# Kernel tuning notes

Hardware: AMD Instinct MI355X
Metric: run time of the kernel (lower is better)

## Reference

```python
import jax, jax.numpy as jnp
import numpy as np

EPS = 1e-6
H = 16

def setup_inputs() -> dict:
    key = jax.random.key(0)
    ks = jax.random.split(key, 11)
    B, L, D = 4, 4096, 1024
    sc = 1.0 / np.sqrt(D)
    return {
        "queries": jax.random.normal(ks[0], (B, L, D), jnp.float32),
        "keys": jax.random.normal(ks[1], (B, L, D), jnp.float32),
        "values": jax.random.normal(ks[2], (B, L, D), jnp.float32),
        "Wq": jax.random.normal(ks[3], (D, D), jnp.float32) * sc,
        "bq": jax.random.normal(ks[4], (D,), jnp.float32) * 0.01,
        "Wk": jax.random.normal(ks[5], (D, D), jnp.float32) * sc,
        "bk": jax.random.normal(ks[6], (D,), jnp.float32) * 0.01,
        "Wv": jax.random.normal(ks[7], (D, D), jnp.float32) * sc,
        "bv": jax.random.normal(ks[8], (D,), jnp.float32) * 0.01,
        "Wo": jax.random.normal(ks[9], (D, D), jnp.float32) * sc,
        "bo": jax.random.normal(ks[10], (D,), jnp.float32) * 0.01,
    }

def reference(queries, keys, values, Wq, bq, Wk, bk, Wv, bv, Wo, bo):
    B, L, _ = queries.shape
    S = keys.shape[1]
    # projections + split heads: [B, H, L, dh]
    q = (queries @ Wq + bq).reshape(B, L, H, -1).transpose(0, 2, 1, 3)
    k = (keys @ Wk + bk).reshape(B, S, H, -1).transpose(0, 2, 1, 3)
    v = (values @ Wv + bv).reshape(B, S, H, -1).transpose(0, 2, 1, 3)
    # kernel feature map
    q = jax.nn.sigmoid(q)
    k = jax.nn.sigmoid(k)
    # flow normalization (sink/source)
    sink_incoming = 1.0 / jnp.einsum('nhld,nhd->nhl', q + EPS, k.sum(axis=2) + EPS)
    source_outgoing = 1.0 / jnp.einsum('nhld,nhd->nhl', k + EPS, q.sum(axis=2) + EPS)
    conserved_sink = jnp.einsum('nhld,nhd->nhl', q + EPS,
                                (k * source_outgoing[..., None]).sum(axis=2) + EPS)
    conserved_source = jnp.einsum('nhld,nhd->nhl', k + EPS,
                                  (q * sink_incoming[..., None]).sum(axis=2) + EPS)
    conserved_source = jnp.clip(conserved_source, -1.0, 1.0)
    sink_allocation = jax.nn.sigmoid(conserved_sink * (float(L) / float(S)))
    source_competition = jax.nn.softmax(conserved_source, axis=-1) * float(S)
    # linear attention: kv then q(kv)
    qn = q * sink_incoming[..., None]
    vn = v * source_competition[..., None]
    kv = jnp.einsum('nhld,nhlm->nhdm', k, vn)
    x = jnp.einsum('nhld,nhdm->nhlm', qn, kv) * sink_allocation[..., None]
    x = x.transpose(0, 2, 1, 3).reshape(B, L, -1)
    return x @ Wo + bo
```

## Files before the change

### kernel.cpp

```cpp
#include <hip/hip_runtime.h>

#define Bc 4
#define Lc 4096
#define Dc 1024
#define LDQ 3072
#define Mc (Bc*Lc)
#define EPSc 1e-6f

typedef __bf16 bf16x8 __attribute__((ext_vector_type(8)));
typedef __bf16 bf16x4 __attribute__((ext_vector_type(4)));
typedef float f32x4 __attribute__((ext_vector_type(4)));

typedef __attribute__((address_space(3))) void lds_vt;
typedef const __attribute__((address_space(1))) void gbl_vt;

__device__ __forceinline__ void gll16(const void* g, void* l) {
  __builtin_amdgcn_global_load_lds((gbl_vt*)g, (lds_vt*)l, 16, 0, 0);
}

__global__ __launch_bounds__(256) void conv3(const float* __restrict__ Q, const float* __restrict__ K,
                                             const float* __restrict__ V, __bf16* __restrict__ Y) {
  const float* src = (blockIdx.y == 0) ? Q : (blockIdx.y == 1) ? K : V;
  __bf16* dst = Y + (size_t)blockIdx.y * ((size_t)Mc * Dc);
  const int i = blockIdx.x * 256 + threadIdx.x;
  const float4 v = ((const float4*)src)[i];
  bf16x4 o;
  o[0] = (__bf16)v.x; o[1] = (__bf16)v.y; o[2] = (__bf16)v.z; o[3] = (__bf16)v.w;
  ((bf16x4*)dst)[i] = o;
}

__global__ __launch_bounds__(256) void wt_conv4(const float* __restrict__ W0, const float* __restrict__ W1,
                                                const float* __restrict__ W2, const float* __restrict__ W3,
                                                __bf16* __restrict__ T) {
  const float* W = (blockIdx.z == 0) ? W0 : (blockIdx.z == 1) ? W1 : (blockIdx.z == 2) ? W2 : W3;
  __bf16* Wt = T + (size_t)blockIdx.z * ((size_t)Dc * Dc);
  __shared__ float t[32][33];
  const int n0 = blockIdx.x << 5, k0 = blockIdx.y << 5;
  const int tx = threadIdx.x, ty = threadIdx.y;
#pragma unroll
  for (int i = 0; i < 4; ++i)
    t[ty + 8 * i][tx] = W[(size_t)(k0 + ty + 8 * i) * Dc + n0 + tx];
  __syncthreads();
#pragma unroll
  for (int i = 0; i < 4; ++i)
    Wt[(size_t)(n0 + ty + 8 * i) * Dc + k0 + tx] = (__bf16)t[tx][ty + 8 * i];
}

template <int FUSED>
__global__ __launch_bounds__(256, 2) void gemm256x128(
    const __bf16* __restrict__ Aq_, const __bf16* __restrict__ Ak_, const __bf16* __restrict__ Av_,
    const __bf16* __restrict__ Wq_, const __bf16* __restrict__ Wk_, const __bf16* __restrict__ Wv_,
    const float* __restrict__ bq_, const float* __restrict__ bk_, const float* __restrict__ bv_,
    void* __restrict__ Cp, float* __restrict__ qsum, float* __restrict__ ksum) {
  __shared__ __bf16 As[256 * 32];
  __shared__ __bf16 Bs[128 * 32];
  const int tid = threadIdx.x;
  const int lane = tid & 63, w4 = tid >> 6;
  const int wr = w4 >> 1, wc = w4 & 1;
  const int lf = lane & 15, kq = lane >> 4;

  constexpr int NCT = FUSED ? 24 : 8;
  constexpr int CPX = (64 * NCT) >> 3;
  const int hwlin = blockIdx.x + blockIdx.y * 64;
  const int swz = (hwlin & 7) * CPX + (hwlin >> 3);
  const int bx = swz / NCT, ct = swz - bx * NCT;
  const int row0 = bx << 8, col0 = ct << 7;
  const int region = FUSED ? (ct >> 3) : 0;
  const int colL = FUSED ? (col0 & 1023) : col0;

  const __bf16* Agl = FUSED ? (region == 0 ? Aq_ : (region == 1 ? Ak_ : Av_)) : Aq_;
  const __bf16* Bgl = FUSED ? (region == 0 ? Wq_ : (region == 1 ? Wk_ : Wv_)) : Wq_;
  const float* biasp = FUSED ? (region == 0 ? bq_ : (region == 1 ? bk_ : bv_)) : bq_;
  const __bf16* Ab_g = Agl + (size_t)row0 * 1024;
  const __bf16* Bb_g = Bgl + (size_t)colL * 1024;

  int arow[4], asrc[4];
#pragma unroll
  for (int i = 0; i < 4; ++i) {
    const int g = i * 256 + tid;
    arow[i] = g >> 2;
    asrc[i] = ((g & 3) ^ ((arow[i] >> 1) & 3)) << 3;
  }
  const int kgsw = (kq ^ ((lf >> 1) & 3)) << 3;
  const int arb = (wr * 128 + lf) * 32 + kgsw;
  const int brb = (wc * 64 + lf) * 32 + kgsw;

  f32x4 acc[8][4] = {};

  for (int t = 0; t < 32; ++t) {
    const int kb = t << 5;
#pragma unroll
    for (int i = 0; i < 4; ++i)
      gll16(Ab_g + (size_t)arow[i] * 1024 + kb + asrc[i], &As[(i * 256 + tid) * 8]);
#pragma unroll
    for (int i = 0; i < 2; ++i)
      gll16(Bb_g + (size_t)arow[i] * 1024 + kb + asrc[i], &Bs[(i * 256 + tid) * 8]);
    __syncthreads();
    bf16x8 af[8], bfr[4];
#pragma unroll
    for (int m = 0; m < 8; ++m) af[m] = *(const bf16x8*)(As + arb + m * 512);
#pragma unroll
    for (int n = 0; n < 4; ++n) bfr[n] = *(const bf16x8*)(Bs + brb + n * 512);
#pragma unroll
    for (int m = 0; m < 8; ++m)
#pragma unroll
      for (int n = 0; n < 4; ++n)
        acc[m][n] = __builtin_amdgcn_mfma_f32_16x16x32_bf16(bfr[n], af[m], acc[m][n], 0, 0, 0);
    __syncthreads();
  }

  const int b_of = row0 >> 12;
  const int orow = row0 + wr * 128 + lf;
  const int ocl = wc * 64 + (kq << 2);
#pragma unroll
  for (int n = 0; n < 4; ++n) {
    const int cl = ocl + (n << 4);
    const int cb = colL + cl;
    const f32x4 bb = *(const f32x4*)&biasp[cb];
    f32x4 sacc = {0.f, 0.f, 0.f, 0.f};
#pragma unroll
    for (int m = 0; m < 8; ++m) {
      f32x4 v = acc[m][n] + bb;
      if (FUSED && region < 2) {
#pragma unroll
        for (int r = 0; r < 4; ++r) v[r] = 1.0f / (1.0f + expf(-v[r]));
      }
      if (FUSED) {
        bf16x4 o;
#pragma unroll
        for (int r = 0; r < 4; ++r) o[r] = (__bf16)v[r];
        *(bf16x4*)&((__bf16*)Cp)[(size_t)(orow + (m << 4)) * LDQ + col0 + cl] = o;
      } else {
        *(f32x4*)&((float*)Cp)[(size_t)(orow + (m << 4)) * 1024 + col0 + cl] = v;
      }
      sacc += v;
    }
    if (FUSED && region < 2) {
#pragma unroll
      for (int o = 1; o < 16; o <<= 1) {
        sacc[0] += __shfl_xor(sacc[0], o); sacc[1] += __shfl_xor(sacc[1], o);
        sacc[2] += __shfl_xor(sacc[2], o); sacc[3] += __shfl_xor(sacc[3], o);
      }
      if (lf == 0) {
        float* sums = (region == 0) ? qsum : ksum;
#pragma unroll
        for (int r = 0; r < 4; ++r) atomicAdd(&sums[b_of * 1024 + cb + r], sacc[r]);
      }
    }
  }
}

__global__ __launch_bounds__(256) void r2_flow(const __bf16* __restrict__ Qp, const __bf16* __restrict__ Kp,
                                               const float* __restrict__ ksum, const float* __restrict__ qsum,
                                               float* __restrict__ si,
                                               float* __restrict__ qsi, float* __restrict__ kso) {
  const int blk = blockIdx.x;
  const int chunk = blk & 15, bh = blk >> 4;
  const int b = bh >> 4, h = bh & 15;
  const int d = threadIdx.x & 63, w = threadIdx.x >> 6;
  __shared__ float ksE[64], qsE[64];
  if (threadIdx.x < 64) ksE[threadIdx.x] = ksum[bh * 64 + threadIdx.x] + EPSc;
  else if (threadIdx.x < 128) qsE[threadIdx.x - 64] = qsum[bh * 64 + threadIdx.x - 64] + EPSc;
  __syncthreads();
  const float kE = ksE[d], qE = qsE[d];
  const size_t base = ((size_t)b * Lc) * LDQ + h * 64 + d;
  const size_t obase = (size_t)bh * Lc;
  float qsia = 0.f, ksoa = 0.f;
  const int l0 = chunk * 256;
  for (int i = w; i < 256; i += 4) {
    const int l = l0 + i;
    const size_t idx = base + (size_t)l * LDQ;
    const float qv = (float)Qp[idx], kvv = (float)Kp[idx];
    float a = (qv + EPSc) * kE;
    float c2 = (kvv + EPSc) * qE;
#pragma unroll
    for (int o = 32; o; o >>= 1) { a += __shfl_xor(a, o); c2 += __shfl_xor(c2, o); }
    const float sil = 1.0f / a, sol = 1.0f / c2;
    if (d == 0) si[obase + l] = sil;
    qsia += qv * sil;
    ksoa += kvv * sol;
  }
  atomicAdd(&qsi[bh * 64 + d], qsia);
  atomicAdd(&kso[bh * 64 + d], ksoa);
}

__global__ __launch_bounds__(256) void r3_cons(const __bf16* __restrict__ Qp, const __bf16* __restrict__ Kp,
                                               const float* __restrict__ qsi, const float* __restrict__ kso,
                                               float* __restrict__ sa, float* __restrict__ csx,
                                               float* __restrict__ den) {
  const int blk = blockIdx.x;
  const int chunk = blk & 15, bh = blk >> 4;
  const int b = bh >> 4, h = bh & 15;
  const int d = threadIdx.x & 63, w = threadIdx.x >> 6;
  __shared__ float ksoE[64], qsiE[64];
  if (threadIdx.x < 64) ksoE[threadIdx.x] = kso[bh * 64 + threadIdx.x] + EPSc;
  else if (threadIdx.x < 128) qsiE[threadIdx.x - 64] = qsi[bh * 64 + threadIdx.x - 64] + EPSc;
  __syncthreads();
  const float kE = ksoE[d], qE = qsiE[d];
  const size_t base = ((size_t)b * Lc) * LDQ + h * 64 + d;
  const size_t obase = (size_t)bh * Lc;
  const int l0 = chunk * 256;
  float eacc = 0.f;
  for (int i = w; i < 256; i += 4) {
    const int l = l0 + i;
    const size_t idx = base + (size_t)l * LDQ;
    const float qv = (float)Qp[idx], kvv = (float)Kp[idx];
    float a = (qv + EPSc) * kE;
    float c2 = (kvv + EPSc) * qE;
#pragma unroll
    for (int o = 32; o; o >>= 1) { a += __shfl_xor(a, o); c2 += __shfl_xor(c2, o); }
    if (d == 0) {
      sa[obase + l] = 1.0f / (1.0f + expf(-a));
      const float cl = fminf(1.0f, fmaxf(-1.0f, c2));
      const float e = expf(cl);
      csx[obase + l] = e;
      eacc += e;
    }
  }
  if (d == 0) atomicAdd(&den[bh], eacc);
}

__global__ __launch_bounds__(256) void k5_kv(const __bf16* __restrict__ Kp, const __bf16* __restrict__ Vp,
                                             const float* __restrict__ csx, const float* __restrict__ den,
                                             float* __restrict__ kvout) {
  const int bh = blockIdx.x, chunk = blockIdx.y;
  const int b = bh >> 4, h = bh & 15;
  const int tid = threadIdx.x;
  const int dq = (tid >> 4) << 2;
  const int mq = (tid & 15) << 2;
  const float sden = 4096.0f / den[bh];
  __shared__ float klds[4][64], vlds[4][64];
  float acc[4][4] = {};
  const int r = tid >> 6, c = tid & 63;
  const size_t rowbase = ((size_t)b * Lc + chunk * 512) * LDQ + h * 64;
  const size_t csbase = (size_t)bh * Lc + chunk * 512;
  for (int i = 0; i < 512; i += 4) {
    const size_t idx = rowbase + (size_t)(i + r) * LDQ + c;
    const float sc = csx[csbase + i + r] * sden;
    klds[r][c] = (float)Kp[idx];
    vlds[r][c] = (float)Vp[idx] * sc;
    __syncthreads();
#pragma unroll
    for (int rr = 0; rr < 4; ++rr) {
      float kr[4], vr[4];
#pragma unroll
      for (int j = 0; j < 4; ++j) { kr[j] = klds[rr][dq + j]; vr[j] = vlds[rr][mq + j]; }
#pragma unroll
      for (int a = 0; a < 4; ++a)
#pragma unroll
        for (int e = 0; e < 4; ++e) acc[a][e] += kr[a] * vr[e];
    }
    __syncthreads();
  }
#pragma unroll
  for (int a = 0; a < 4; ++a)
#pragma unroll
    for (int e = 0; e < 4; ++e)
      atomicAdd(&kvout[(size_t)bh * 4096 + (dq + a) * 64 + mq + e], acc[a][e]);
}

__global__ __launch_bounds__(256) void k6_x(const __bf16* __restrict__ Qp,
                                            const float* __restrict__ kvin, const float* __restrict__ si,
                                            const float* __restrict__ sa, __bf16* __restrict__ Xb) {
  const int bh = blockIdx.x, chunk = blockIdx.y;
  const int b = bh >> 4, h = bh & 15;
  const int tid = threadIdx.x, lane = tid & 63, w = tid >> 6;
  const int lf = lane & 15, kq = lane >> 4;
  __shared__ float ktl[64][66];
  for (int e = tid; e < 4096; e += 256)
    ktl[e & 63][e >> 6] = kvin[(size_t)bh * 4096 + e];
  __syncthreads();
  bf16x8 kh[4][2], kl[4][2];
#pragma unroll
  for (int mi = 0; mi < 4; ++mi)
#pragma unroll
    for (int hf = 0; hf < 2; ++hf) {
      const float* p = &ktl[mi * 16 + lf][hf * 32 + kq * 8];
      bf16x8 hi, lo;
#pragma unroll
      for (int j = 0; j < 8; ++j) {
        const float f = p[j];
        hi[j] = (__bf16)f;
        lo[j] = (__bf16)(f - (float)hi[j]);
      }
      kh[mi][hf] = hi; kl[mi][hf] = lo;
    }
  const size_t bL = (size_t)b * Lc;
  const size_t obase = (size_t)bh * Lc;
#pragma unroll
  for (int gi = 0; gi < 4; ++gi) {
    const int lrow = chunk * 256 + (w * 4 + gi) * 16 + lf;
    const size_t qb = (bL + lrow) * LDQ + h * 64;
    const bf16x8 qf0 = *(const bf16x8*)(Qp + qb + kq * 8);
    const bf16x8 qf1 = *(const bf16x8*)(Qp + qb + 32 + kq * 8);
    const float sc = si[obase + lrow] * sa[obase + lrow];
    f32x4 acc[4] = {};
#pragma unroll
    for (int mi = 0; mi < 4; ++mi) {
      acc[mi] = __builtin_amdgcn_mfma_f32_16x16x32_bf16(kh[mi][0], qf0, acc[mi], 0, 0, 0);
      acc[mi] = __builtin_amdgcn_mfma_f32_16x16x32_bf16(kh[mi][1], qf1, acc[mi], 0, 0, 0);
      acc[mi] = __builtin_amdgcn_mfma_f32_16x16x32_bf16(kl[mi][0], qf0, acc[mi], 0, 0, 0);
      acc[mi] = __builtin_amdgcn_mfma_f32_16x16x32_bf16(kl[mi][1], qf1, acc[mi], 0, 0, 0);
    }
#pragma unroll
    for (int mi = 0; mi < 4; ++mi) {
      bf16x4 o;
#pragma unroll
      for (int r = 0; r < 4; ++r) o[r] = (__bf16)(acc[mi][r] * sc);
      *(bf16x4*)&Xb[(bL + lrow) * Dc + h * 64 + mi * 16 + (kq << 2)] = o;
    }
  }
}

extern "C" void kernel_launch(void* const* d_in, const int* in_sizes, int n_in,
                              void* d_out, int out_size, void* d_ws, size_t ws_size,
                              hipStream_t stream) {
  const float* Qin = (const float*)d_in[0];
  const float* Kin = (const float*)d_in[1];
  const float* Vin = (const float*)d_in[2];
  const float* Wq = (const float*)d_in[3];
  const float* bq = (const float*)d_in[4];
  const float* Wk = (const float*)d_in[5];
  const float* bk = (const float*)d_in[6];
  const float* Wv = (const float*)d_in[7];
  const float* bv = (const float*)d_in[8];
  const float* Wo = (const float*)d_in[9];
  const float* bo = (const float*)d_in[10];

  const size_t MD = (size_t)Mc * Dc;
  __bf16* Aq = (__bf16*)d_ws;
  __bf16* Ak = Aq + MD;
  __bf16* Av = Ak + MD;
  __bf16* Wqt = Av + MD;
  __bf16* Wkt = Wqt + (size_t)Dc * Dc;
  __bf16* Wvt = Wkt + (size_t)Dc * Dc;
  __bf16* Wot = Wvt + (size_t)Dc * Dc;
  __bf16* QKV = Wot + (size_t)Dc * Dc;
  float* F = (float*)(QKV + (size_t)Mc * LDQ);
  float* ksum = F;
  float* qsum = ksum + 4096;
  float* kso = qsum + 4096;
  float* qsi = kso + 4096;
  float* den = qsi + 4096;
  float* kv = den + 64;
  float* si = kv + 262144;
  float* sa = si + 262144;
  float* csx = sa + 262144;
  __bf16* Xb = Aq;

  hipMemsetAsync(F, 0, (size_t)(4 * 4096 + 64 + 262144) * sizeof(float), stream);

  conv3<<<dim3((int)(MD / 4 / 256), 3), 256, 0, stream>>>(Qin, Kin, Vin, Aq);
  wt_conv4<<<dim3(32, 32, 4), dim3(32, 8), 0, stream>>>(Wq, Wk, Wv, Wo, Wqt);

  gemm256x128<1><<<dim3(64, 24), 256, 0, stream>>>(Aq, Ak, Av, Wqt, Wkt, Wvt,
                                                   bq, bk, bv, QKV, qsum, ksum);

  const __bf16* Qp = QKV;
  const __bf16* Kp = QKV + 1024;
  const __bf16* Vp = QKV + 2048;
  r2_flow<<<1024, 256, 0, stream>>>(Qp, Kp, ksum, qsum, si, qsi, kso);
  r3_cons<<<1024, 256, 0, stream>>>(Qp, Kp, qsi, kso, sa, csx, den);
  k5_kv<<<dim3(64, 8), 256, 0, stream>>>(Kp, Vp, csx, den, kv);
  k6_x<<<dim3(64, 16), 256, 0, stream>>>(Qp, kv, si, sa, Xb);

  gemm256x128<0><<<dim3(64, 8), 256, 0, stream>>>(Xb, nullptr, nullptr, Wot, nullptr, nullptr,
                                                  bo, nullptr, nullptr, d_out, nullptr, nullptr);
}
```

Baseline: 490.6 us.

## Use 128x128 tiles with 64-wide K steps for fused QKV projection GEMM

Adds a new GEMM kernel with 128x128 output tiles and a 64-deep K step per loop iteration, loaded as two 32-wide LDS halves, with a launch bound of 4 blocks per CU. The fused QKV projection now uses it instead of the 256x128 kernel. The grid doubles to 3072 blocks and each iteration issues more loads per barrier, aiming at higher occupancy, better wave balance across CUs and fewer syncs. The trade-off is less operand reuse per block and twice as many atomic column-sum updates.

```diff
diff --git a/kernel.cpp b/kernel.cpp
--- a/kernel.cpp
+++ b/kernel.cpp
@@ -44,6 +44,116 @@
 #pragma unroll
   for (int i = 0; i < 4; ++i)
     Wt[(size_t)(n0 + ty + 8 * i) * Dc + k0 + tx] = (__bf16)t[tx][ty + 8 * i];
+}
+
+template <int FUSED>
+__global__ __launch_bounds__(256, 4) void gemm128b(
+    const __bf16* __restrict__ Aq_, const __bf16* __restrict__ Ak_, const __bf16* __restrict__ Av_,
+    const __bf16* __restrict__ Wq_, const __bf16* __restrict__ Wk_, const __bf16* __restrict__ Wv_,
+    const float* __restrict__ bq_, const float* __restrict__ bk_, const float* __restrict__ bv_,
+    void* __restrict__ Cp, float* __restrict__ qsum, float* __restrict__ ksum) {
+  __shared__ __bf16 As[2][128 * 32];
+  __shared__ __bf16 Bs[2][128 * 32];
+  const int tid = threadIdx.x;
+  const int lane = tid & 63, w4 = tid >> 6;
+  const int wr = w4 >> 1, wc = w4 & 1;
+  const int lf = lane & 15, kq = lane >> 4;
+
+  constexpr int NCT = FUSED ? 24 : 8;
+  constexpr int CPX = (128 * NCT) >> 3;
+  const int hwlin = blockIdx.x + (blockIdx.y << 7);
+  const int swz = (hwlin & 7) * CPX + (hwlin >> 3);
+  const int bx = swz / NCT, ct = swz - bx * NCT;
+  const int row0 = bx << 7, col0 = ct << 7;
+  const int region = FUSED ? (ct >> 3) : 0;
+  const int colL = FUSED ? (col0 & 1023) : col0;
+
+  const __bf16* Agl = FUSED ? (region == 0 ? Aq_ : (region == 1 ? Ak_ : Av_)) : Aq_;
+  const __bf16* Bgl = FUSED ? (region == 0 ? Wq_ : (region == 1 ? Wk_ : Wv_)) : Wq_;
+  const float* biasp = FUSED ? (region == 0 ? bq_ : (region == 1 ? bk_ : bv_)) : bq_;
+  const __bf16* Ab_g = Agl + (size_t)row0 * 1024;
+  const __bf16* Bb_g = Bgl + (size_t)colL * 1024;
+
+  const int srow = (w4 << 5) + (lane >> 2);
+  const int sgd = lane & 3;
+  const int ssrc = (sgd ^ ((lane >> 3) & 3)) << 3;
+  const size_t aoff0 = (size_t)srow * 1024 + ssrc;
+  const size_t aoff1 = (size_t)(srow + 16) * 1024 + ssrc;
+  const int ldst0 = srow * 32 + (sgd << 3);
+  const int ldst1 = (srow + 16) * 32 + (sgd << 3);
+
+  const int kgsw = (kq ^ ((lf >> 1) & 3)) << 3;
+  const int arb = (wr * 64 + lf) * 32 + kgsw;
+  const int brb = (wc * 64 + lf) * 32 + kgsw;
+
+  f32x4 acc[4][4] = {};
+
+  for (int t = 0; t < 16; ++t) {
+    const int kb = t << 6;
+    gll16(Ab_g + aoff0 + kb, &As[0][ldst0]);
+    gll16(Ab_g + aoff1 + kb, &As[0][ldst1]);
+    gll16(Bb_g + aoff0 + kb, &Bs[0][ldst0]);
+    gll16(Bb_g + aoff1 + kb, &Bs[0][ldst1]);
+    gll16(Ab_g + aoff0 + kb + 32, &As[1][ldst0]);
+    gll16(Ab_g + aoff1 + kb + 32, &As[1][ldst1]);
+    gll16(Bb_g + aoff0 + kb + 32, &Bs[1][ldst0]);
+    gll16(Bb_g + aoff1 + kb + 32, &Bs[1][ldst1]);
+    __syncthreads();
+#pragma unroll
+    for (int hf = 0; hf < 2; ++hf) {
+      bf16x8 af[4], bfr[4];
+#pragma unroll
+      for (int m = 0; m < 4; ++m) af[m] = *(const bf16x8*)(&As[hf][0] + arb + m * 512);
+#pragma unroll
+      for (int n = 0; n < 4; ++n) bfr[n] = *(const bf16x8*)(&Bs[hf][0] + brb + n * 512);
+#pragma unroll
+      for (int m = 0; m < 4; ++m)
+#pragma unroll
+        for (int n = 0; n < 4; ++n)
+          acc[m][n] = __builtin_amdgcn_mfma_f32_16x16x32_bf16(bfr[n], af[m], acc[m][n], 0, 0, 0);
+    }
+    __syncthreads();
+  }
+
+  const int b_of = row0 >> 12;
+  const int orow = row0 + wr * 64 + lf;
+  const int ocl = wc * 64 + (kq << 2);
+#pragma unroll
+  for (int n = 0; n < 4; ++n) {
+    const int cl = ocl + (n << 4);
+    const int cb = colL + cl;
+    const f32x4 bb = *(const f32x4*)&biasp[cb];
+    f32x4 sacc = {0.f, 0.f, 0.f, 0.f};
+#pragma unroll
+    for (int m = 0; m < 4; ++m) {
+      f32x4 v = acc[m][n] + bb;
+      if (FUSED && region < 2) {
+#pragma unroll
+        for (int r = 0; r < 4; ++r) v[r] = 1.0f / (1.0f + expf(-v[r]));
+      }
+      if (FUSED) {
+        bf16x4 o;
+#pragma unroll
+        for (int r = 0; r < 4; ++r) o[r] = (__bf16)v[r];
+        *(bf16x4*)&((__bf16*)Cp)[(size_t)(orow + (m << 4)) * LDQ + col0 + cl] = o;
+      } else {
+        *(f32x4*)&((float*)Cp)[(size_t)(orow + (m << 4)) * 1024 + col0 + cl] = v;
+      }
+      sacc += v;
+    }
+    if (FUSED && region < 2) {
+#pragma unroll
+      for (int o = 1; o < 16; o <<= 1) {
+        sacc[0] += __shfl_xor(sacc[0], o); sacc[1] += __shfl_xor(sacc[1], o);
+        sacc[2] += __shfl_xor(sacc[2], o); sacc[3] += __shfl_xor(sacc[3], o);
+      }
+      if (lf == 0) {
+        float* sums = (region == 0) ? qsum : ksum;
+#pragma unroll
+        for (int r = 0; r < 4; ++r) atomicAdd(&sums[b_of * 1024 + cb + r], sacc[r]);
+      }
+    }
+  }
 }
 
 template <int FUSED>
@@ -353,8 +463,8 @@
   conv3<<<dim3((int)(MD / 4 / 256), 3), 256, 0, stream>>>(Qin, Kin, Vin, Aq);
   wt_conv4<<<dim3(32, 32, 4), dim3(32, 8), 0, stream>>>(Wq, Wk, Wv, Wo, Wqt);
 
-  gemm256x128<1><<<dim3(64, 24), 256, 0, stream>>>(Aq, Ak, Av, Wqt, Wkt, Wvt,
-                                                   bq, bk, bv, QKV, qsum, ksum);
+  gemm128b<1><<<dim3(128, 24), 256, 0, stream>>>(Aq, Ak, Av, Wqt, Wkt, Wvt,
+                                                 bq, bk, bv, QKV, qsum, ksum);
 
   const __bf16* Qp = QKV;
   const __bf16* Kp = QKV + 1024;
```

Result: no change. 497.2 us (+1.3%).

## Fuse conservation pass into kv and x kernels, defer softmax normalization

Applied to the files above, without the earlier changes.

Removes the separate r3_cons kernel. The conserved-source exponent is now computed inside k5_kv, which also accumulates the softmax denominator. The conserved-sink sigmoid is recomputed inside k6_x from the Q fragments it already loads. The 4096/den scaling moves from V to the final x scale, which is algebraically equivalent because kv is linear in V. k5_kv now stages 16 rows per sync instead of 4, and the GEMM launch bounds ask for 4 waves per SIMD, which may force register spills.

```diff
diff --git a/kernel.cpp b/kernel.cpp
--- a/kernel.cpp
+++ b/kernel.cpp
@@ -47,7 +47,7 @@
 }
 
 template <int FUSED>
-__global__ __launch_bounds__(256, 2) void gemm256x128(
+__global__ __launch_bounds__(256, 4) void gemm256x128(
     const __bf16* __restrict__ Aq_, const __bf16* __restrict__ Ak_, const __bf16* __restrict__ Av_,
     const __bf16* __restrict__ Wq_, const __bf16* __restrict__ Wk_, const __bf16* __restrict__ Wv_,
     const float* __restrict__ bq_, const float* __restrict__ bk_, const float* __restrict__ bv_,
@@ -184,88 +184,79 @@
   atomicAdd(&kso[bh * 64 + d], ksoa);
 }
 
-__global__ __launch_bounds__(256) void r3_cons(const __bf16* __restrict__ Qp, const __bf16* __restrict__ Kp,
-                                               const float* __restrict__ qsi, const float* __restrict__ kso,
-                                               float* __restrict__ sa, float* __restrict__ csx,
-                                               float* __restrict__ den) {
-  const int blk = blockIdx.x;
-  const int chunk = blk & 15, bh = blk >> 4;
-  const int b = bh >> 4, h = bh & 15;
-  const int d = threadIdx.x & 63, w = threadIdx.x >> 6;
-  __shared__ float ksoE[64], qsiE[64];
-  if (threadIdx.x < 64) ksoE[threadIdx.x] = kso[bh * 64 + threadIdx.x] + EPSc;
-  else if (threadIdx.x < 128) qsiE[threadIdx.x - 64] = qsi[bh * 64 + threadIdx.x - 64] + EPSc;
-  __syncthreads();
-  const float kE = ksoE[d], qE = qsiE[d];
-  const size_t base = ((size_t)b * Lc) * LDQ + h * 64 + d;
-  const size_t obase = (size_t)bh * Lc;
-  const int l0 = chunk * 256;
-  float eacc = 0.f;
-  for (int i = w; i < 256; i += 4) {
-    const int l = l0 + i;
-    const size_t idx = base + (size_t)l * LDQ;
-    const float qv = (float)Qp[idx], kvv = (float)Kp[idx];
-    float a = (qv + EPSc) * kE;
-    float c2 = (kvv + EPSc) * qE;
-#pragma unroll
-    for (int o = 32; o; o >>= 1) { a += __shfl_xor(a, o); c2 += __shfl_xor(c2, o); }
-    if (d == 0) {
-      sa[obase + l] = 1.0f / (1.0f + expf(-a));
-      const float cl = fminf(1.0f, fmaxf(-1.0f, c2));
-      const float e = expf(cl);
-      csx[obase + l] = e;
-      eacc += e;
-    }
-  }
-  if (d == 0) atomicAdd(&den[bh], eacc);
-}
-
 __global__ __launch_bounds__(256) void k5_kv(const __bf16* __restrict__ Kp, const __bf16* __restrict__ Vp,
-                                             const float* __restrict__ csx, const float* __restrict__ den,
+                                             const float* __restrict__ qsi, float* __restrict__ den,
                                              float* __restrict__ kvout) {
   const int bh = blockIdx.x, chunk = blockIdx.y;
   const int b = bh >> 4, h = bh & 15;
   const int tid = threadIdx.x;
   const int dq = (tid >> 4) << 2;
   const int mq = (tid & 15) << 2;
-  const float sden = 4096.0f / den[bh];
-  __shared__ float klds[4][64], vlds[4][64];
+  __shared__ float qsE[64];
+  __shared__ float klds[16][64], vlds[16][64];
+  if (tid < 64) qsE[tid] = qsi[bh * 64 + tid] + EPSc;
+  __syncthreads();
   float acc[4][4] = {};
-  const int r = tid >> 6, c = tid & 63;
+  float eacc = 0.f;
+  const int w = tid >> 6, c = tid & 63;
+  const float qE = qsE[c];
   const size_t rowbase = ((size_t)b * Lc + chunk * 512) * LDQ + h * 64;
-  const size_t csbase = (size_t)bh * Lc + chunk * 512;
-  for (int i = 0; i < 512; i += 4) {
-    const size_t idx = rowbase + (size_t)(i + r) * LDQ + c;
-    const float sc = csx[csbase + i + r] * sden;
-    klds[r][c] = (float)Kp[idx];
-    vlds[r][c] = (float)Vp[idx] * sc;
+  for (int i = 0; i < 32; ++i) {
+    float kvf[4], vpe[4];
+#pragma unroll
+    for (int rr = 0; rr < 4; ++rr) {
+      const int lrow = i * 16 + rr * 4 + w;
+      const size_t idx = rowbase + (size_t)lrow * LDQ + c;
+      kvf[rr] = (float)Kp[idx];
+      const float vvf = (float)Vp[idx];
+      float c2 = (kvf[rr] + EPSc) * qE;
+#pragma unroll
+      for (int o = 32; o; o >>= 1) c2 += __shfl_xor(c2, o);
+      const float e = expf(fminf(1.0f, fmaxf(-1.0f, c2)));
+      if (c == 0) eacc += e;
+      vpe[rr] = vvf * e;
+    }
     __syncthreads();
 #pragma unroll
     for (int rr = 0; rr < 4; ++rr) {
+      klds[rr * 4 + w][c] = kvf[rr];
+      vlds[rr * 4 + w][c] = vpe[rr];
+    }
+    __syncthreads();
+#pragma unroll
+    for (int rr = 0; rr < 16; ++rr) {
       float kr[4], vr[4];
 #pragma unroll
       for (int j = 0; j < 4; ++j) { kr[j] = klds[rr][dq + j]; vr[j] = vlds[rr][mq + j]; }
 #pragma unroll
       for (int a = 0; a < 4; ++a)
 #pragma unroll
-        for (int e = 0; e < 4; ++e) acc[a][e] += kr[a] * vr[e];
-    }
-    __syncthreads();
-  }
+        for (int e2 = 0; e2 < 4; ++e2) acc[a][e2] += kr[a] * vr[e2];
+    }
+  }
+  if (c == 0) atomicAdd(&den[bh], eacc);
 #pragma unroll
   for (int a = 0; a < 4; ++a)
 #pragma unroll
-    for (int e = 0; e < 4; ++e)
-      atomicAdd(&kvout[(size_t)bh * 4096 + (dq + a) * 64 + mq + e], acc[a][e]);
+    for (int e2 = 0; e2 < 4; ++e2)
+      atomicAdd(&kvout[(size_t)bh * 4096 + (dq + a) * 64 + mq + e2], acc[a][e2]);
 }
 
 __global__ __launch_bounds__(256) void k6_x(const __bf16* __restrict__ Qp,
                                             const float* __restrict__ kvin, const float* __restrict__ si,
-                                            const float* __restrict__ sa, __bf16* __restrict__ Xb) {
+                                            const float* __restrict__ kso, const float* __restrict__ den,
+                                            __bf16* __restrict__ Xb) {
   const int bh = blockIdx.x, chunk = blockIdx.y;
   const int b = bh >> 4, h = bh & 15;
   const int tid = threadIdx.x, lane = tid & 63, w = tid >> 6;
   const int lf = lane & 15, kq = lane >> 4;
+  const float sden = 4096.0f / den[bh];
+  f32x4 kE0a = *(const f32x4*)&kso[bh * 64 + kq * 8];
+  f32x4 kE0b = *(const f32x4*)&kso[bh * 64 + kq * 8 + 4];
+  f32x4 kE1a = *(const f32x4*)&kso[bh * 64 + 32 + kq * 8];
+  f32x4 kE1b = *(const f32x4*)&kso[bh * 64 + 32 + kq * 8 + 4];
+#pragma unroll
+  for (int j = 0; j < 4; ++j) { kE0a[j] += EPSc; kE0b[j] += EPSc; kE1a[j] += EPSc; kE1b[j] += EPSc; }
   __shared__ float ktl[64][66];
   for (int e = tid; e < 4096; e += 256)
     ktl[e & 63][e >> 6] = kvin[(size_t)bh * 4096 + e];
@@ -293,7 +284,18 @@
     const size_t qb = (bL + lrow) * LDQ + h * 64;
     const bf16x8 qf0 = *(const bf16x8*)(Qp + qb + kq * 8);
     const bf16x8 qf1 = *(const bf16x8*)(Qp + qb + 32 + kq * 8);
-    const float sc = si[obase + lrow] * sa[obase + lrow];
+    float a = 0.f;
+#pragma unroll
+    for (int j = 0; j < 4; ++j) {
+      a += ((float)qf0[j] + EPSc) * kE0a[j];
+      a += ((float)qf0[4 + j] + EPSc) * kE0b[j];
+      a += ((float)qf1[j] + EPSc) * kE1a[j];
+      a += ((float)qf1[4 + j] + EPSc) * kE1b[j];
+    }
+    a += __shfl_xor(a, 16);
+    a += __shfl_xor(a, 32);
+    const float sav = 1.0f / (1.0f + expf(-a));
+    const float sc = si[obase + lrow] * sav * sden;
     f32x4 acc[4] = {};
 #pragma unroll
     for (int mi = 0; mi < 4; ++mi) {
@@ -344,8 +346,6 @@
   float* den = qsi + 4096;
   float* kv = den + 64;
   float* si = kv + 262144;
-  float* sa = si + 262144;
-  float* csx = sa + 262144;
   __bf16* Xb = Aq;
 
   hipMemsetAsync(F, 0, (size_t)(4 * 4096 + 64 + 262144) * sizeof(float), stream);
@@ -360,9 +360,8 @@
   const __bf16* Kp = QKV + 1024;
   const __bf16* Vp = QKV + 2048;
   r2_flow<<<1024, 256, 0, stream>>>(Qp, Kp, ksum, qsum, si, qsi, kso);
-  r3_cons<<<1024, 256, 0, stream>>>(Qp, Kp, qsi, kso, sa, csx, den);
-  k5_kv<<<dim3(64, 8), 256, 0, stream>>>(Kp, Vp, csx, den, kv);
-  k6_x<<<dim3(64, 16), 256, 0, stream>>>(Qp, kv, si, sa, Xb);
+  k5_kv<<<dim3(64, 8), 256, 0, stream>>>(Kp, Vp, qsi, den, kv);
+  k6_x<<<dim3(64, 16), 256, 0, stream>>>(Qp, kv, si, kso, den, Xb);
 
   gemm256x128<0><<<dim3(64, 8), 256, 0, stream>>>(Xb, nullptr, nullptr, Wot, nullptr, nullptr,
                                                   bo, nullptr, nullptr, d_out, nullptr, nullptr);
```

After: 1.201 ms. 145% more time.
